# Optimization experiments

Measured on AMD Instinct MI355X. Metric: run time of the kernel, lower is better.

## Reference

```python
import jax, jax.numpy as jnp
import numpy as np

D_HIDN = 768
N_HEAD = 12
D_HEAD = 64
LN_EPS = 1e-5


def setup_inputs() -> dict:
    key = jax.random.key(0)
    ks = jax.random.split(key, 16)
    B, S, D = 4, 2048, D_HIDN
    s = 0.02
    inputs = jax.random.normal(ks[0], (B, S, D), dtype=jnp.float32)
    attn_mask = jax.random.uniform(ks[1], (B, S, S)) < 0.1
    Wq = jax.random.normal(ks[2], (D, D), jnp.float32) * s
    bq = jnp.zeros((D,), jnp.float32)
    Wk = jax.random.normal(ks[3], (D, D), jnp.float32) * s
    bk = jnp.zeros((D,), jnp.float32)
    Wv = jax.random.normal(ks[4], (D, D), jnp.float32) * s
    bv = jnp.zeros((D,), jnp.float32)
    g1 = jnp.ones((D,), jnp.float32)
    beta1 = jnp.zeros((D,), jnp.float32)
    W1 = jax.random.normal(ks[5], (D, 4 * D), jnp.float32) * s
    b1 = jnp.zeros((4 * D,), jnp.float32)
    W2 = jax.random.normal(ks[6], (4 * D, D), jnp.float32) * s
    b2 = jnp.zeros((D,), jnp.float32)
    g2 = jnp.ones((D,), jnp.float32)
    beta2 = jnp.zeros((D,), jnp.float32)
    return dict(inputs=inputs, attn_mask=attn_mask, Wq=Wq, bq=bq, Wk=Wk, bk=bk,
                Wv=Wv, bv=bv, g1=g1, beta1=beta1, W1=W1, b1=b1, W2=W2, b2=b2,
                g2=g2, beta2=beta2)


def _layernorm(x, g, b):
    mu = jnp.mean(x, axis=-1, keepdims=True)
    var = jnp.mean(jnp.square(x - mu), axis=-1, keepdims=True)
    return (x - mu) * jax.lax.rsqrt(var + LN_EPS) * g + b


def reference(inputs, attn_mask, Wq, bq, Wk, bk, Wv, bv, g1, beta1,
              W1, b1, W2, b2, g2, beta2):
    B, S, D = inputs.shape
    H, Dh = N_HEAD, D_HEAD
    # QKV projections -> [B, H, S, Dh]
    q = (inputs @ Wq + bq).reshape(B, S, H, Dh).transpose(0, 2, 1, 3)
    k = (inputs @ Wk + bk).reshape(B, S, H, Dh).transpose(0, 2, 1, 3)
    v = (inputs @ Wv + bv).reshape(B, S, H, Dh).transpose(0, 2, 1, 3)
    scale = 1.0 / (Dh ** 0.5)
    scores = jnp.einsum('bhqd,bhkd->bhqk', q, k) * scale  # [B,H,S,S]
    scores = jnp.where(attn_mask[:, None, :, :], jnp.float32(-1e9), scores)
    attn = jax.nn.softmax(scores, axis=-1)
    ctx = jnp.einsum('bhqk,bhkd->bhqd', attn, v)  # [B,H,S,Dh]
    attn_out = ctx.transpose(0, 2, 1, 3).reshape(B, S, D)
    # Add & Norm 1
    ffn_in = _layernorm(attn_out + inputs, g1, beta1)
    # FFN (note: no activation in the original module)
    ffn_out = (ffn_in @ W1 + b1) @ W2 + b2
    # Add & Norm 2
    return _layernorm(ffn_out + ffn_in, g2, beta2)
```

## Files before the change

### kernel.cpp

```cpp
#include <hip/hip_runtime.h>

typedef unsigned short u16;
typedef __attribute__((ext_vector_type(8))) __bf16 bf16x8;
typedef __attribute__((ext_vector_type(4))) __bf16 bf16x4;
typedef __attribute__((ext_vector_type(4))) float f32x4;

#define DEV __device__ __forceinline__

DEV u16 f2bf(float f) {
  unsigned u = __builtin_bit_cast(unsigned, f);
  u += 0x7FFFu + ((u >> 16) & 1u);
  return (u16)(u >> 16);
}
DEV float bf2f(u16 u) {
  unsigned v = (unsigned)u << 16;
  return __builtin_bit_cast(float, v);
}

DEV void stage16(const void* g, void* l) {
  __builtin_amdgcn_global_load_lds((const __attribute__((address_space(1))) void*)g,
                                   (__attribute__((address_space(3))) void*)l, 16, 0, 0);
}

DEV f32x4 mfma32(bf16x8 a, bf16x8 b, f32x4 c) {
  return __builtin_amdgcn_mfma_f32_16x16x32_bf16(a, b, c, 0, 0, 0);
}

DEV void transpose_tile(const float* __restrict__ src, u16* __restrict__ dst,
                        int R, int C, int bx, int by, int t, float (*tile)[33]) {
  int tx = t & 31, ty = t >> 5;
  int c0 = bx * 32, r0 = by * 32;
#pragma unroll
  for (int i = 0; i < 4; ++i)
    tile[ty + i * 8][tx] = src[(size_t)(r0 + ty + i * 8) * C + c0 + tx];
  __syncthreads();
#pragma unroll
  for (int i = 0; i < 4; ++i)
    dst[(size_t)(c0 + ty + i * 8) * R + r0 + tx] = f2bf(tile[tx][ty + i * 8]);
}

__global__ __launch_bounds__(256) void prep_all(
    const float* __restrict__ Wq, const float* __restrict__ Wk, const float* __restrict__ Wv,
    const float* __restrict__ W1, const float* __restrict__ W2,
    const float* __restrict__ inputs, const int* __restrict__ maskI,
    u16* __restrict__ WqkvT, u16* __restrict__ W1b, u16* __restrict__ W2T,
    u16* __restrict__ Xb, unsigned long long* __restrict__ bits) {
  __shared__ float tile[32][33];
  const int t = threadIdx.x;
  const int bid = blockIdx.x;
  if (bid < 1728) {
    int z = bid / 576, rem = bid % 576;
    const float* src = (z == 0) ? Wq : (z == 1 ? Wk : Wv);
    transpose_tile(src, WqkvT + (size_t)z * 768 * 768, 768, 768, rem % 24, rem / 24, t, tile);
  } else if (bid < 4032) {
    int rem = bid - 1728;
    transpose_tile(W2, W2T, 3072, 768, rem % 24, rem / 24, t, tile);
  } else if (bid < 6336) {
    int i = (bid - 4032) * 256 + t;
    float4 f = ((const float4*)W1)[i];
    ushort4 u;
    u.x = f2bf(f.x); u.y = f2bf(f.y); u.z = f2bf(f.z); u.w = f2bf(f.w);
    ((ushort4*)W1b)[i] = u;
  } else if (bid < 12480) {
    int i = (bid - 6336) * 256 + t;
    float4 f = ((const float4*)inputs)[i];
    ushort4 u;
    u.x = f2bf(f.x); u.y = f2bf(f.y); u.z = f2bf(f.z); u.w = f2bf(f.w);
    ((ushort4*)Xb)[i] = u;
  } else {
    int lb = bid - 12480;
    int lane = t & 63;
    int w0 = (lb * 4 + (t >> 6)) * 4;
#pragma unroll
    for (int j = 0; j < 4; ++j) {
      int v = maskI[(size_t)(w0 + j) * 64 + lane];
      unsigned long long bm = __ballot(v != 0);
      if (lane == 0) bits[w0 + j] = bm;
    }
  }
}

template <int MODE>
DEV void gemm_body(u16 (*Als)[128 * 32], u16 (*Bls)[128 * 32],
                   const u16* __restrict__ A, const u16* __restrict__ Bt, int K,
                   const float* __restrict__ b0, const float* __restrict__ b1p,
                   const float* __restrict__ b2p, const u16* __restrict__ resid,
                   u16* __restrict__ outQ, u16* __restrict__ outK, u16* __restrict__ outV,
                   float* __restrict__ outP, int bx, int by, int bz) {
  const int t = threadIdx.x;
  const int lane = t & 63, wv = t >> 6;
  const int wm = wv & 1, wn = wv >> 1;
  const int lrow = lane & 15, g = lane >> 4;
  const int m0 = by * 128, n0 = bx * 128;

  int koff = 0, klen = K;
  if (MODE == 2) { klen = K >> 1; koff = bz * klen; }
  if (MODE == 4) { klen = K >> 2; koff = bz * klen; }

  f32x4 acc[4][4] = {};

  const int idx0 = t, idx1 = 256 + t;
  const int row0 = idx0 >> 2, sl0 = (idx0 & 3) ^ ((row0 >> 1) & 3);
  const int row1 = idx1 >> 2, sl1 = (idx1 & 3) ^ ((row1 >> 1) & 3);

  auto stage = [&](int k0, int buf) {
    stage16(A + (size_t)(m0 + row0) * K + koff + k0 + sl0 * 8, (char*)Als[buf] + idx0 * 16);
    stage16(Bt + (size_t)(n0 + row0) * K + koff + k0 + sl0 * 8, (char*)Bls[buf] + idx0 * 16);
    stage16(A + (size_t)(m0 + row1) * K + koff + k0 + sl1 * 8, (char*)Als[buf] + idx1 * 16);
    stage16(Bt + (size_t)(n0 + row1) * K + koff + k0 + sl1 * 8, (char*)Bls[buf] + idx1 * 16);
  };

  stage(0, 0);
  __syncthreads();

  int nk = klen >> 5;
  for (int it = 0; it < nk; ++it) {
    int cur = it & 1;
    if (it + 1 < nk) stage((it + 1) << 5, cur ^ 1);
    bf16x8 af[4], bfr[4];
#pragma unroll
    for (int mi = 0; mi < 4; ++mi) {
      int r = wm * 64 + mi * 16 + lrow;
      int sl = g ^ ((r >> 1) & 3);
      af[mi] = *(const bf16x8*)((const char*)Als[cur] + r * 64 + sl * 16);
    }
#pragma unroll
    for (int ni = 0; ni < 4; ++ni) {
      int r = wn * 64 + ni * 16 + lrow;
      int sl = g ^ ((r >> 1) & 3);
      bfr[ni] = *(const bf16x8*)((const char*)Bls[cur] + r * 64 + sl * 16);
    }
    __builtin_amdgcn_s_setprio(1);
#pragma unroll
    for (int mi = 0; mi < 4; ++mi)
#pragma unroll
      for (int ni = 0; ni < 4; ++ni)
        acc[mi][ni] = mfma32(af[mi], bfr[ni], acc[mi][ni]);
    __builtin_amdgcn_s_setprio(0);
    __syncthreads();
  }

#pragma unroll
  for (int mi = 0; mi < 4; ++mi)
#pragma unroll
    for (int ni = 0; ni < 4; ++ni)
#pragma unroll
      for (int reg = 0; reg < 4; ++reg) {
        int gm = m0 + wm * 64 + mi * 16 + g * 4 + reg;
        int gn = n0 + wn * 64 + ni * 16 + lrow;
        float v = acc[mi][ni][reg];
        if (MODE == 0) {
          int p = gn / 768, nn = gn - p * 768;
          const float* bb = (p == 0) ? b0 : (p == 1 ? b1p : b2p);
          v += bb[nn];
          int b = gm >> 11, s = gm & 2047;
          int h = nn >> 6, dh = nn & 63;
          size_t hh = (size_t)(b * 12 + h);
          if (p == 0)      outQ[(hh * 2048 + s) * 64 + dh] = f2bf(v * 0.1803368801f);
          else if (p == 1) outK[(hh * 2048 + s) * 64 + dh] = f2bf(v);
          else             outV[(hh * 64 + dh) * 2048 + s] = f2bf(v);
        } else if (MODE == 2) {
          if (bz == 1) {
            v += b0[gn] + bf2f(resid[(size_t)gm * 768 + gn]);
            outK[(size_t)gm * 768 + gn] = f2bf(v);
          } else {
            outQ[(size_t)gm * 768 + gn] = f2bf(v);
          }
        } else {
          outP[(size_t)gn * 768 + gm] = v;
        }
      }
}

template <int MODE, int OCC>
__global__ __launch_bounds__(256, OCC) void gemm_k(
    const u16* __restrict__ A, const u16* __restrict__ Bt, int K,
    const float* __restrict__ b0, const u16* __restrict__ resid,
    u16* __restrict__ out0, u16* __restrict__ out1) {
  __shared__ u16 Als[2][128 * 32];
  __shared__ u16 Bls[2][128 * 32];
  gemm_body<MODE>(Als, Bls, A, Bt, K, b0, nullptr, nullptr, resid,
                  out0, out1, nullptr, nullptr, blockIdx.x, blockIdx.y, blockIdx.z);
}

__global__ __launch_bounds__(256, 4) void fused_gemms(
    const u16* __restrict__ Xb, const u16* __restrict__ WqkvT,
    const float* __restrict__ bq, const float* __restrict__ bk, const float* __restrict__ bv,
    u16* __restrict__ Qb, u16* __restrict__ Kb, u16* __restrict__ Vtb,
    const u16* __restrict__ W1b, const u16* __restrict__ W2T, float* __restrict__ W12P,
    const float* __restrict__ b1, const float* __restrict__ b2, float* __restrict__ biasEff) {
  __shared__ u16 Als[2][128 * 32];
  __shared__ u16 Bls[2][128 * 32];
  const int bid = blockIdx.x;
  if (bid < 144) {
    int z = bid / 36, tl = bid % 36;
    gemm_body<4>(Als, Bls, W1b, W2T, 3072, nullptr, nullptr, nullptr, nullptr,
                 nullptr, nullptr, nullptr, W12P + (size_t)z * 768 * 768,
                 tl % 6, tl / 6, z);
  } else if (bid < 1296) {
    int lb = bid - 144;
    gemm_body<0>(Als, Bls, Xb, WqkvT, 768, bq, bk, bv, nullptr,
                 Qb, Kb, Vtb, nullptr, lb % 18, lb / 18, 0);
  } else {
    const int j = bid - 1296, t = threadIdx.x;
    float* red = (float*)Als;
    float s = 0.f;
    for (int k = t; k < 3072; k += 256) s += b1[k] * bf2f(W2T[(size_t)j * 3072 + k]);
    for (int d = 1; d < 64; d <<= 1) s += __shfl_xor(s, d, 64);
    if ((t & 63) == 0) red[t >> 6] = s;
    __syncthreads();
    if (t == 0) biasEff[j] = b2[j] + red[0] + red[1] + red[2] + red[3];
  }
}

__global__ __launch_bounds__(512, 6) void attn_fwd(
    const u16* __restrict__ Q, const u16* __restrict__ Kg, const u16* __restrict__ Vt,
    const unsigned long long* __restrict__ mbits, u16* __restrict__ attn_out) {
  __shared__ u16 Kls[2][64 * 64];
  __shared__ u16 Vls[2][64 * 64];
  __shared__ u16 Pls[8][16 * 64];
  const int t = threadIdx.x, lane = t & 63, wv = t >> 6;
  const int lrow = lane & 15, g = lane >> 4;

  const int fid = blockIdx.x;
  const int swz = (fid & 7) * 96 + (fid >> 3);
  const int bh = swz >> 4, q0 = (swz & 15) * 128;
  const int b = bh / 12, h = bh % 12;
  const u16* Qh = Q + (size_t)bh * 2048 * 64;
  const u16* Kh = Kg + (size_t)bh * 2048 * 64;
  const u16* Vh = Vt + (size_t)bh * 64 * 2048;

  const int qr = q0 + wv * 16 + lrow;
  bf16x8 aq[2];
  aq[0] = *(const bf16x8*)(Qh + (size_t)qr * 64 + g * 8);
  aq[1] = *(const bf16x8*)(Qh + (size_t)qr * 64 + 32 + g * 8);

  bf16x8 ones;
#pragma unroll
  for (int j = 0; j < 8; ++j) ones[j] = (__bf16)1.0f;

  f32x4 acc[4] = {};
  f32x4 lacc = {};

  const int row0 = t >> 3, sl0 = (t & 7) ^ (row0 & 7);
  auto stage = [&](int kt, int buf) {
    stage16(Kh + ((size_t)(kt * 64 + row0)) * 64 + sl0 * 8, (char*)Kls[buf] + t * 16);
    stage16(Vh + (size_t)row0 * 2048 + kt * 64 + sl0 * 8, (char*)Vls[buf] + t * 16);
  };

  const unsigned long long* mrow = mbits + ((size_t)b * 2048 + qr) * 32;
  unsigned long long mb = mrow[0];

  stage(0, 0);
  __syncthreads();

#pragma unroll 2
  for (int kt = 0; kt < 32; ++kt) {
    const int cur = kt & 1;
    if (kt + 1 < 32) stage(kt + 1, cur ^ 1);

    f32x4 sc[4];
#pragma unroll
    for (int c = 0; c < 4; ++c) {
      sc[c] = 0.f;
#pragma unroll
      for (int ks = 0; ks < 2; ++ks) {
        int r = c * 16 + lrow;
        int sl = (ks * 4 + g) ^ (r & 7);
        bf16x8 bk = *(const bf16x8*)((const char*)Kls[cur] + r * 128 + sl * 16);
        sc[c] = mfma32(bk, aq[ks], sc[c]);
      }
    }

    unsigned long long mbn = (kt + 1 < 32) ? mrow[kt + 1] : 0;

    unsigned mlo = (unsigned)mb, mhi = (unsigned)(mb >> 32);
#pragma unroll
    for (int c = 0; c < 4; ++c) {
      unsigned bits = ((c & 2) ? mhi : mlo) >> ((c & 1) * 16 + 4 * g);
#pragma unroll
      for (int reg = 0; reg < 4; ++reg)
        sc[c][reg] = ((bits >> reg) & 1) ? 0.f : __builtin_amdgcn_exp2f(sc[c][reg]);
    }
    mb = mbn;

#pragma unroll
    for (int c = 0; c < 4; ++c) {
      bf16x4 pk;
#pragma unroll
      for (int reg = 0; reg < 4; ++reg) pk[reg] = (__bf16)sc[c][reg];
      int slot = 2 * c + (g >> 1);
      int byte = lrow * 128 + ((slot ^ (lrow & 7)) << 4) + (g & 1) * 8;
      *(bf16x4*)((char*)Pls[wv] + byte) = pk;
    }
    asm volatile("s_waitcnt lgkmcnt(0)" ::: "memory");

#pragma unroll
    for (int ks = 0; ks < 2; ++ks) {
      int slp = (ks * 4 + g) ^ (lrow & 7);
      bf16x8 pa = *(const bf16x8*)((const char*)Pls[wv] + lrow * 128 + slp * 16);
      lacc = mfma32(pa, ones, lacc);
#pragma unroll
      for (int c = 0; c < 4; ++c) {
        int r = c * 16 + lrow;
        int sl = (ks * 4 + g) ^ (r & 7);
        bf16x8 vf = *(const bf16x8*)((const char*)Vls[cur] + r * 128 + sl * 16);
        acc[c] = mfma32(pa, vf, acc[c]);
      }
    }
    __syncthreads();
  }

  float rl[4];
#pragma unroll
  for (int reg = 0; reg < 4; ++reg) rl[reg] = 1.0f / lacc[reg];
#pragma unroll
  for (int c = 0; c < 4; ++c)
#pragma unroll
    for (int reg = 0; reg < 4; ++reg) {
      int q = q0 + wv * 16 + 4 * g + reg;
      int col = h * 64 + c * 16 + lrow;
      attn_out[((size_t)b * 2048 + q) * 768 + col] = f2bf(acc[c][reg] * rl[reg]);
    }
}

__global__ __launch_bounds__(192) void ln_fused2(
    const u16* __restrict__ x1b, const u16* __restrict__ x2b,
    const float* __restrict__ gam, const float* __restrict__ bet,
    float* __restrict__ outf, u16* __restrict__ outb,
    const float* __restrict__ W12P, u16* __restrict__ W12T, int nrows) {
  const int row = blockIdx.x, t = threadIdx.x;
  if (row >= nrows) {
    const int i = (row - nrows) * 192 + t;
    float4 s = ((const float4*)W12P)[i];
#pragma unroll
    for (int z = 1; z < 4; ++z) {
      float4 q = ((const float4*)(W12P + (size_t)z * 768 * 768))[i];
      s.x += q.x; s.y += q.y; s.z += q.z; s.w += q.w;
    }
    ushort4 u;
    u.x = f2bf(s.x); u.y = f2bf(s.y); u.z = f2bf(s.z); u.w = f2bf(s.w);
    ((ushort4*)W12T)[i] = u;
    return;
  }
  const size_t base = (size_t)row * 768 + t * 4;
  bf16x4 a = *(const bf16x4*)(x1b + base);
  bf16x4 c = *(const bf16x4*)(x2b + base);
  float v[4], s = 0.f;
#pragma unroll
  for (int j = 0; j < 4; ++j) { v[j] = (float)a[j] + (float)c[j]; s += v[j]; }
  __shared__ float red[3];
  for (int d = 1; d < 64; d <<= 1) s += __shfl_xor(s, d, 64);
  if ((t & 63) == 0) red[t >> 6] = s;
  __syncthreads();
  s = red[0] + red[1] + red[2];
  float mu = s * (1.f / 768.f);
  float sq = 0.f;
#pragma unroll
  for (int j = 0; j < 4; ++j) { float d = v[j] - mu; sq += d * d; }
  __syncthreads();
  for (int d = 1; d < 64; d <<= 1) sq += __shfl_xor(sq, d, 64);
  if ((t & 63) == 0) red[t >> 6] = sq;
  __syncthreads();
  sq = red[0] + red[1] + red[2];
  float rs = rsqrtf(sq * (1.f / 768.f) + 1e-5f);
  const int i0 = t * 4;
  float y[4];
#pragma unroll
  for (int j = 0; j < 4; ++j) y[j] = (v[j] - mu) * rs * gam[i0 + j] + bet[i0 + j];
  if (outf) {
    float4 o = make_float4(y[0], y[1], y[2], y[3]);
    *(float4*)(outf + base) = o;
  }
  if (outb) {
    ushort4 u;
    u.x = f2bf(y[0]); u.y = f2bf(y[1]); u.z = f2bf(y[2]); u.w = f2bf(y[3]);
    *(ushort4*)(outb + base) = u;
  }
}

extern "C" void kernel_launch(void* const* d_in, const int* in_sizes, int n_in,
                              void* d_out, int out_size, void* d_ws, size_t ws_size,
                              hipStream_t stream) {
  const float* inputs = (const float*)d_in[0];
  const int*   maskI  = (const int*)d_in[1];
  const float* Wq = (const float*)d_in[2];  const float* bq = (const float*)d_in[3];
  const float* Wk = (const float*)d_in[4];  const float* bk = (const float*)d_in[5];
  const float* Wv = (const float*)d_in[6];  const float* bv = (const float*)d_in[7];
  const float* g1 = (const float*)d_in[8];  const float* be1 = (const float*)d_in[9];
  const float* W1 = (const float*)d_in[10]; const float* b1 = (const float*)d_in[11];
  const float* W2 = (const float*)d_in[12]; const float* b2 = (const float*)d_in[13];
  const float* g2 = (const float*)d_in[14]; const float* be2 = (const float*)d_in[15];
  float* out = (float*)d_out;

  char* w = (char*)d_ws;
  auto take = [&](size_t n) { char* p = w; w += (n + 255) & ~(size_t)255; return p; };
  u16* WqkvT = (u16*)take((size_t)2304 * 768 * 2);
  u16* W1b   = (u16*)take((size_t)768 * 3072 * 2);
  u16* W2T   = (u16*)take((size_t)768 * 3072 * 2);
  u16* W12T  = (u16*)take((size_t)768 * 768 * 2);
  float* W12P = (float*)take((size_t)4 * 768 * 768 * 4);
  float* biasEff = (float*)take((size_t)768 * 4);
  u16* Xb    = (u16*)take((size_t)8192 * 768 * 2);
  u16* Qb    = (u16*)take((size_t)48 * 2048 * 64 * 2);
  u16* Kb    = (u16*)take((size_t)48 * 2048 * 64 * 2);
  u16* Vtb   = (u16*)take((size_t)48 * 64 * 2048 * 2);
  unsigned long long* mbits = (unsigned long long*)take((size_t)4 * 2048 * 32 * 8);
  u16*   attnB   = (u16*)take((size_t)8192 * 768 * 2);
  u16*   ffnB    = (u16*)take((size_t)8192 * 768 * 2);
  if ((size_t)(w - (char*)d_ws) > ws_size) return;
  u16* pre0b = Qb;
  u16* pre1b = Kb;

  prep_all<<<28864, 256, 0, stream>>>(Wq, Wk, Wv, W1, W2, inputs, maskI,
                                      WqkvT, W1b, W2T, Xb, mbits);
  fused_gemms<<<2064, 256, 0, stream>>>(Xb, WqkvT, bq, bk, bv, Qb, Kb, Vtb,
                                        W1b, W2T, W12P, b1, b2, biasEff);
  attn_fwd<<<768, 512, 0, stream>>>(Qb, Kb, Vtb, mbits, attnB);
  ln_fused2<<<8960, 192, 0, stream>>>(attnB, Xb, g1, be1, nullptr, ffnB,
                                      W12P, W12T, 8192);
  gemm_k<2, 4><<<dim3(6, 64, 2), 256, 0, stream>>>(ffnB, W12T, 768, biasEff, ffnB,
                                                   pre0b, pre1b);
  ln_fused2<<<8192, 192, 0, stream>>>(pre0b, pre1b, g2, be2, out, nullptr,
                                      nullptr, nullptr, 8192);
}
```

Before: 236.5 us.

## Double per-wave query rows in attention and move bias folding into layernorm launch

The attention kernel now runs 256 threads per block, with each wave handling 32 query rows as two 16-row halves. Each K and V fragment read from LDS therefore feeds two MFMAs, which halves LDS traffic per unit of compute. The cost is more registers per thread, which the occupancy hint of 3 reflects, and two staging loads per thread for each tile. Separately, the b1·W2 effective-bias reduction moves out of the fused GEMM launch into extra blocks of the first layernorm launch, which runs before biasEff is consumed.

Measured after the change: 240.9 us. Within noise of the previous version (+1.9%).

```diff
diff --git a/kernel.cpp b/kernel.cpp
--- a/kernel.cpp
+++ b/kernel.cpp
@@ -187,8 +187,7 @@
     const u16* __restrict__ Xb, const u16* __restrict__ WqkvT,
     const float* __restrict__ bq, const float* __restrict__ bk, const float* __restrict__ bv,
     u16* __restrict__ Qb, u16* __restrict__ Kb, u16* __restrict__ Vtb,
-    const u16* __restrict__ W1b, const u16* __restrict__ W2T, float* __restrict__ W12P,
-    const float* __restrict__ b1, const float* __restrict__ b2, float* __restrict__ biasEff) {
+    const u16* __restrict__ W1b, const u16* __restrict__ W2T, float* __restrict__ W12P) {
   __shared__ u16 Als[2][128 * 32];
   __shared__ u16 Bls[2][128 * 32];
   const int bid = blockIdx.x;
@@ -197,28 +196,19 @@
     gemm_body<4>(Als, Bls, W1b, W2T, 3072, nullptr, nullptr, nullptr, nullptr,
                  nullptr, nullptr, nullptr, W12P + (size_t)z * 768 * 768,
                  tl % 6, tl / 6, z);
-  } else if (bid < 1296) {
+  } else {
     int lb = bid - 144;
     gemm_body<0>(Als, Bls, Xb, WqkvT, 768, bq, bk, bv, nullptr,
                  Qb, Kb, Vtb, nullptr, lb % 18, lb / 18, 0);
-  } else {
-    const int j = bid - 1296, t = threadIdx.x;
-    float* red = (float*)Als;
-    float s = 0.f;
-    for (int k = t; k < 3072; k += 256) s += b1[k] * bf2f(W2T[(size_t)j * 3072 + k]);
-    for (int d = 1; d < 64; d <<= 1) s += __shfl_xor(s, d, 64);
-    if ((t & 63) == 0) red[t >> 6] = s;
-    __syncthreads();
-    if (t == 0) biasEff[j] = b2[j] + red[0] + red[1] + red[2] + red[3];
-  }
-}
-
-__global__ __launch_bounds__(512, 6) void attn_fwd(
+  }
+}
+
+__global__ __launch_bounds__(256, 3) void attn_fwd(
     const u16* __restrict__ Q, const u16* __restrict__ Kg, const u16* __restrict__ Vt,
     const unsigned long long* __restrict__ mbits, u16* __restrict__ attn_out) {
   __shared__ u16 Kls[2][64 * 64];
   __shared__ u16 Vls[2][64 * 64];
-  __shared__ u16 Pls[8][16 * 64];
+  __shared__ u16 Pls[4][32 * 64];
   const int t = threadIdx.x, lane = t & 63, wv = t >> 6;
   const int lrow = lane & 15, g = lane >> 4;
 
@@ -230,106 +220,146 @@
   const u16* Kh = Kg + (size_t)bh * 2048 * 64;
   const u16* Vh = Vt + (size_t)bh * 64 * 2048;
 
-  const int qr = q0 + wv * 16 + lrow;
-  bf16x8 aq[2];
-  aq[0] = *(const bf16x8*)(Qh + (size_t)qr * 64 + g * 8);
-  aq[1] = *(const bf16x8*)(Qh + (size_t)qr * 64 + 32 + g * 8);
+  const int qr0 = q0 + wv * 32 + lrow;
+  bf16x8 aq[2][2];
+#pragma unroll
+  for (int qh = 0; qh < 2; ++qh) {
+    aq[qh][0] = *(const bf16x8*)(Qh + (size_t)(qr0 + qh * 16) * 64 + g * 8);
+    aq[qh][1] = *(const bf16x8*)(Qh + (size_t)(qr0 + qh * 16) * 64 + 32 + g * 8);
+  }
 
   bf16x8 ones;
 #pragma unroll
   for (int j = 0; j < 8; ++j) ones[j] = (__bf16)1.0f;
 
-  f32x4 acc[4] = {};
-  f32x4 lacc = {};
-
-  const int row0 = t >> 3, sl0 = (t & 7) ^ (row0 & 7);
+  f32x4 acc[2][4] = {};
+  f32x4 lacc[2] = {};
+
+  const int idx0 = t, idx1 = 256 + t;
+  const int row0 = idx0 >> 3, sl0 = (idx0 & 7) ^ (row0 & 7);
+  const int row1 = idx1 >> 3, sl1 = (idx1 & 7) ^ (row1 & 7);
   auto stage = [&](int kt, int buf) {
-    stage16(Kh + ((size_t)(kt * 64 + row0)) * 64 + sl0 * 8, (char*)Kls[buf] + t * 16);
-    stage16(Vh + (size_t)row0 * 2048 + kt * 64 + sl0 * 8, (char*)Vls[buf] + t * 16);
+    stage16(Kh + ((size_t)(kt * 64 + row0)) * 64 + sl0 * 8, (char*)Kls[buf] + idx0 * 16);
+    stage16(Vh + (size_t)row0 * 2048 + kt * 64 + sl0 * 8, (char*)Vls[buf] + idx0 * 16);
+    stage16(Kh + ((size_t)(kt * 64 + row1)) * 64 + sl1 * 8, (char*)Kls[buf] + idx1 * 16);
+    stage16(Vh + (size_t)row1 * 2048 + kt * 64 + sl1 * 8, (char*)Vls[buf] + idx1 * 16);
   };
 
-  const unsigned long long* mrow = mbits + ((size_t)b * 2048 + qr) * 32;
-  unsigned long long mb = mrow[0];
+  const unsigned long long* mr0 = mbits + ((size_t)b * 2048 + qr0) * 32;
+  const unsigned long long* mr1 = mr0 + 16 * 32;
+  unsigned long long mb[2] = {mr0[0], mr1[0]};
 
   stage(0, 0);
   __syncthreads();
 
-#pragma unroll 2
   for (int kt = 0; kt < 32; ++kt) {
     const int cur = kt & 1;
     if (kt + 1 < 32) stage(kt + 1, cur ^ 1);
-
-    f32x4 sc[4];
-#pragma unroll
-    for (int c = 0; c < 4; ++c) {
-      sc[c] = 0.f;
+    const char* Kb = (const char*)Kls[cur];
+    const char* Vb = (const char*)Vls[cur];
+
+    f32x4 sc[2][4];
+#pragma unroll
+    for (int c = 0; c < 4; ++c) { sc[0][c] = 0.f; sc[1][c] = 0.f; }
+#pragma unroll
+    for (int c = 0; c < 4; ++c)
 #pragma unroll
       for (int ks = 0; ks < 2; ++ks) {
         int r = c * 16 + lrow;
         int sl = (ks * 4 + g) ^ (r & 7);
-        bf16x8 bk = *(const bf16x8*)((const char*)Kls[cur] + r * 128 + sl * 16);
-        sc[c] = mfma32(bk, aq[ks], sc[c]);
-      }
-    }
-
-    unsigned long long mbn = (kt + 1 < 32) ? mrow[kt + 1] : 0;
-
-    unsigned mlo = (unsigned)mb, mhi = (unsigned)(mb >> 32);
-#pragma unroll
-    for (int c = 0; c < 4; ++c) {
-      unsigned bits = ((c & 2) ? mhi : mlo) >> ((c & 1) * 16 + 4 * g);
-#pragma unroll
-      for (int reg = 0; reg < 4; ++reg)
-        sc[c][reg] = ((bits >> reg) & 1) ? 0.f : __builtin_amdgcn_exp2f(sc[c][reg]);
-    }
-    mb = mbn;
-
-#pragma unroll
-    for (int c = 0; c < 4; ++c) {
-      bf16x4 pk;
-#pragma unroll
-      for (int reg = 0; reg < 4; ++reg) pk[reg] = (__bf16)sc[c][reg];
-      int slot = 2 * c + (g >> 1);
-      int byte = lrow * 128 + ((slot ^ (lrow & 7)) << 4) + (g & 1) * 8;
-      *(bf16x4*)((char*)Pls[wv] + byte) = pk;
-    }
+        bf16x8 bk = *(const bf16x8*)(Kb + r * 128 + sl * 16);
+        sc[0][c] = mfma32(bk, aq[0][ks], sc[0][c]);
+        sc[1][c] = mfma32(bk, aq[1][ks], sc[1][c]);
+      }
+
+#pragma unroll
+    for (int qh = 0; qh < 2; ++qh) {
+      unsigned mlo = (unsigned)mb[qh], mhi = (unsigned)(mb[qh] >> 32);
+#pragma unroll
+      for (int c = 0; c < 4; ++c) {
+        unsigned bits = ((c & 2) ? mhi : mlo) >> ((c & 1) * 16 + 4 * g);
+#pragma unroll
+        for (int reg = 0; reg < 4; ++reg)
+          sc[qh][c][reg] = ((bits >> reg) & 1) ? 0.f : __builtin_amdgcn_exp2f(sc[qh][c][reg]);
+      }
+    }
+    if (kt + 1 < 32) { mb[0] = mr0[kt + 1]; mb[1] = mr1[kt + 1]; }
+
+#pragma unroll
+    for (int qh = 0; qh < 2; ++qh)
+#pragma unroll
+      for (int c = 0; c < 4; ++c) {
+        bf16x4 pk;
+#pragma unroll
+        for (int reg = 0; reg < 4; ++reg) pk[reg] = (__bf16)sc[qh][c][reg];
+        int slot = 2 * c + (g >> 1);
+        int byte = (qh * 16 + lrow) * 128 + ((slot ^ (lrow & 7)) << 4) + (g & 1) * 8;
+        *(bf16x4*)((char*)Pls[wv] + byte) = pk;
+      }
     asm volatile("s_waitcnt lgkmcnt(0)" ::: "memory");
 
-#pragma unroll
-    for (int ks = 0; ks < 2; ++ks) {
-      int slp = (ks * 4 + g) ^ (lrow & 7);
-      bf16x8 pa = *(const bf16x8*)((const char*)Pls[wv] + lrow * 128 + slp * 16);
-      lacc = mfma32(pa, ones, lacc);
+    bf16x8 pa[2][2];
+#pragma unroll
+    for (int qh = 0; qh < 2; ++qh)
+#pragma unroll
+      for (int ks = 0; ks < 2; ++ks) {
+        int slp = (ks * 4 + g) ^ (lrow & 7);
+        pa[qh][ks] = *(const bf16x8*)((const char*)Pls[wv] + (qh * 16 + lrow) * 128 + slp * 16);
+      }
+#pragma unroll
+    for (int qh = 0; qh < 2; ++qh) {
+      lacc[qh] = mfma32(pa[qh][0], ones, lacc[qh]);
+      lacc[qh] = mfma32(pa[qh][1], ones, lacc[qh]);
+    }
+#pragma unroll
+    for (int ks = 0; ks < 2; ++ks)
 #pragma unroll
       for (int c = 0; c < 4; ++c) {
         int r = c * 16 + lrow;
         int sl = (ks * 4 + g) ^ (r & 7);
-        bf16x8 vf = *(const bf16x8*)((const char*)Vls[cur] + r * 128 + sl * 16);
-        acc[c] = mfma32(pa, vf, acc[c]);
-      }
-    }
+        bf16x8 vf = *(const bf16x8*)(Vb + r * 128 + sl * 16);
+        acc[0][c] = mfma32(pa[0][ks], vf, acc[0][c]);
+        acc[1][c] = mfma32(pa[1][ks], vf, acc[1][c]);
+      }
     __syncthreads();
   }
 
-  float rl[4];
-#pragma unroll
-  for (int reg = 0; reg < 4; ++reg) rl[reg] = 1.0f / lacc[reg];
-#pragma unroll
-  for (int c = 0; c < 4; ++c)
-#pragma unroll
-    for (int reg = 0; reg < 4; ++reg) {
-      int q = q0 + wv * 16 + 4 * g + reg;
-      int col = h * 64 + c * 16 + lrow;
-      attn_out[((size_t)b * 2048 + q) * 768 + col] = f2bf(acc[c][reg] * rl[reg]);
-    }
+  float rl[2][4];
+#pragma unroll
+  for (int qh = 0; qh < 2; ++qh)
+#pragma unroll
+    for (int reg = 0; reg < 4; ++reg) rl[qh][reg] = 1.0f / lacc[qh][reg];
+#pragma unroll
+  for (int qh = 0; qh < 2; ++qh)
+#pragma unroll
+    for (int c = 0; c < 4; ++c)
+#pragma unroll
+      for (int reg = 0; reg < 4; ++reg) {
+        int q = q0 + wv * 32 + qh * 16 + 4 * g + reg;
+        int col = h * 64 + c * 16 + lrow;
+        attn_out[((size_t)b * 2048 + q) * 768 + col] = f2bf(acc[qh][c][reg] * rl[qh][reg]);
+      }
 }
 
 __global__ __launch_bounds__(192) void ln_fused2(
     const u16* __restrict__ x1b, const u16* __restrict__ x2b,
     const float* __restrict__ gam, const float* __restrict__ bet,
     float* __restrict__ outf, u16* __restrict__ outb,
-    const float* __restrict__ W12P, u16* __restrict__ W12T, int nrows) {
+    const float* __restrict__ W12P, u16* __restrict__ W12T, int nrows, int nred,
+    const float* __restrict__ b1, const float* __restrict__ b2,
+    const u16* __restrict__ W2T, float* __restrict__ biasEff) {
   const int row = blockIdx.x, t = threadIdx.x;
+  __shared__ float red[3];
+  if (row >= nrows + nred) {
+    const int j = row - nrows - nred;
+    float s = 0.f;
+    for (int k = t; k < 3072; k += 192) s += b1[k] * bf2f(W2T[(size_t)j * 3072 + k]);
+    for (int d = 1; d < 64; d <<= 1) s += __shfl_xor(s, d, 64);
+    if ((t & 63) == 0) red[t >> 6] = s;
+    __syncthreads();
+    if (t == 0) biasEff[j] = b2[j] + red[0] + red[1] + red[2];
+    return;
+  }
   if (row >= nrows) {
     const int i = (row - nrows) * 192 + t;
     float4 s = ((const float4*)W12P)[i];
@@ -349,7 +379,6 @@
   float v[4], s = 0.f;
 #pragma unroll
   for (int j = 0; j < 4; ++j) { v[j] = (float)a[j] + (float)c[j]; s += v[j]; }
-  __shared__ float red[3];
   for (int d = 1; d < 64; d <<= 1) s += __shfl_xor(s, d, 64);
   if ((t & 63) == 0) red[t >> 6] = s;
   __syncthreads();
@@ -414,13 +443,14 @@
 
   prep_all<<<28864, 256, 0, stream>>>(Wq, Wk, Wv, W1, W2, inputs, maskI,
                                       WqkvT, W1b, W2T, Xb, mbits);
-  fused_gemms<<<2064, 256, 0, stream>>>(Xb, WqkvT, bq, bk, bv, Qb, Kb, Vtb,
-                                        W1b, W2T, W12P, b1, b2, biasEff);
-  attn_fwd<<<768, 512, 0, stream>>>(Qb, Kb, Vtb, mbits, attnB);
-  ln_fused2<<<8960, 192, 0, stream>>>(attnB, Xb, g1, be1, nullptr, ffnB,
-                                      W12P, W12T, 8192);
+  fused_gemms<<<1296, 256, 0, stream>>>(Xb, WqkvT, bq, bk, bv, Qb, Kb, Vtb,
+                                        W1b, W2T, W12P);
+  attn_fwd<<<768, 256, 0, stream>>>(Qb, Kb, Vtb, mbits, attnB);
+  ln_fused2<<<9728, 192, 0, stream>>>(attnB, Xb, g1, be1, nullptr, ffnB,
+                                      W12P, W12T, 8192, 768, b1, b2, W2T, biasEff);
   gemm_k<2, 4><<<dim3(6, 64, 2), 256, 0, stream>>>(ffnB, W12T, 768, biasEff, ffnB,
                                                    pre0b, pre1b);
   ln_fused2<<<8192, 192, 0, stream>>>(pre0b, pre1b, g2, be2, out, nullptr,
-                                      nullptr, nullptr, 8192);
-}
+                                      nullptr, nullptr, 8192, 0,
+                                      nullptr, nullptr, nullptr, nullptr);
+}
```
